# Kernel tuning notes

Hardware: AMD Instinct MI355X
Metric: run time of the kernel (lower is better)

Reference implementation:

```python
import jax, jax.numpy as jnp
import numpy as np
from jax import lax

K = 9
CENTER = K // 2
EXTEND = 1.0
EPS = 1e-5
GROUPS = 16  # out_ch // 4


def conv2d(x, w, b, stride, padding):
    y = lax.conv_general_dilated(x, w, window_strides=stride, padding=padding,
                                 dimension_numbers=('NCHW', 'OIHW', 'NCHW'))
    return y + b[None, :, None, None]


def setup_inputs() -> dict:
    key = jax.random.key(0)
    ks = jax.random.split(key, 9)
    B, C, Wd, Hd, OUT = 8, 64, 128, 128, 64
    f = jax.random.normal(ks[0], (B, C, Wd, Hd), jnp.float32)
    w_off = jax.random.normal(ks[1], (2 * K, C, 3, 3), jnp.float32) * 0.05
    b_off = jax.random.normal(ks[2], (2 * K,), jnp.float32) * 0.05
    bn_gamma = 1.0 + 0.1 * jax.random.normal(ks[3], (2 * K,), jnp.float32)
    bn_beta = 0.1 * jax.random.normal(ks[4], (2 * K,), jnp.float32)
    w_dsc = jax.random.normal(ks[5], (OUT, C, K, 1), jnp.float32) * 0.05
    b_dsc = jax.random.normal(ks[6], (OUT,), jnp.float32) * 0.05
    gn_gamma = 1.0 + 0.1 * jax.random.normal(ks[7], (OUT,), jnp.float32)
    gn_beta = 0.1 * jax.random.normal(ks[8], (OUT,), jnp.float32)
    return {'f': f, 'w_off': w_off, 'b_off': b_off, 'bn_gamma': bn_gamma,
            'bn_beta': bn_beta, 'w_dsc': w_dsc, 'b_dsc': b_dsc,
            'gn_gamma': gn_gamma, 'gn_beta': gn_beta}


def _forward(f, w_off, b_off, bn_gamma, bn_beta, w_dsc, b_dsc, gn_gamma, gn_beta):
    B, C, Wd, Hd = f.shape  # module names: width=shape[2], height=shape[3]
    dt = f.dtype

    # offset branch: conv3x3 -> BatchNorm (training mode, batch stats) -> tanh
    off = conv2d(f, w_off, b_off, (1, 1), 'SAME')
    mu = off.mean(axis=(0, 2, 3), keepdims=True)
    var = off.var(axis=(0, 2, 3), keepdims=True)
    off = (off - mu) / jnp.sqrt(var + EPS)
    off = off * bn_gamma[None, :, None, None] + bn_beta[None, :, None, None]
    off = jnp.tanh(off)

    y_off = off[:, :K]  # [B,K,Wd,Hd]; x_off (off[:, K:]) unused for morph=0

    # cumulative offset scan from the center point (morph=0).
    # NOTE: endpoints 0 and K-1 keep detached raw offsets (torch detach().clone()).
    raw0 = lax.stop_gradient(y_off)
    offn = [None] * K
    offn[CENTER] = jnp.zeros_like(y_off[:, 0])
    for i in range(1, CENTER):
        offn[CENTER + i] = offn[CENTER + i - 1] + y_off[:, CENTER + i]
        offn[CENTER - i] = offn[CENTER - i + 1] + y_off[:, CENTER - i]
    offn[0] = raw0[:, 0]
    offn[K - 1] = raw0[:, K - 1]
    offn = jnp.stack(offn, axis=1)  # [B,K,Wd,Hd]

    # coordinate grids: y indexes the width axis, x the height axis
    y_new = jnp.arange(Wd, dtype=dt)[None, None, :, None] + offn * EXTEND  # [B,K,Wd,Hd]
    x_new = ((jnp.arange(K, dtype=dt) - CENTER)[None, :, None, None]
             + jnp.arange(Hd, dtype=dt)[None, None, None, :])  # [1,K,1,Hd]
    x_new = jnp.broadcast_to(x_new, (B, K, Wd, Hd))

    # layout [B, K*Wd, Hd] via (B,K,Wd,Hd) -> (B,Wd,K,Hd)
    y_s = jnp.transpose(y_new, (0, 2, 1, 3)).reshape(B, K * Wd * Hd)
    x_s = jnp.transpose(x_new, (0, 2, 1, 3)).reshape(B, K * Wd * Hd)

    # bilinear interpolation (clamped corner indices, unclamped y/x in weights)
    y0 = jnp.floor(y_s).astype(jnp.int32)
    x0 = jnp.floor(x_s).astype(jnp.int32)
    y0c = jnp.clip(y0, 0, Wd - 1)
    y1c = jnp.clip(y0 + 1, 0, Wd - 1)
    x0c = jnp.clip(x0, 0, Hd - 1)
    x1c = jnp.clip(x0 + 1, 0, Hd - 1)

    feat = jnp.transpose(f, (0, 2, 3, 1)).reshape(B, Wd * Hd, C)

    def gather(yi, xi):
        idx = (yi * Hd + xi)[:, :, None]  # [B,N,1]
        return jnp.take_along_axis(feat, idx, axis=1)  # [B,N,C]

    va0 = gather(y0c, x0c)
    vc0 = gather(y0c, x1c)
    va1 = gather(y1c, x0c)
    vc1 = gather(y1c, x1c)

    y0f, y1f = y0c.astype(dt), y1c.astype(dt)
    x0f, x1f = x0c.astype(dt), x1c.astype(dt)
    wa = ((y1f - y_s) * (x1f - x_s))[:, :, None]
    wb = ((y1f - y_s) * (x_s - x0f))[:, :, None]
    wc = ((y_s - y0f) * (x1f - x_s))[:, :, None]
    wd = ((y_s - y0f) * (x_s - x0f))[:, :, None]

    out = va0 * wa + vc0 * wb + va1 * wc + vc1 * wd  # [B,N,C]
    deformed = jnp.transpose(out.reshape(B, K * Wd, Hd, C), (0, 3, 1, 2))  # [B,C,K*Wd,Hd]

    # strided conv over the K snake points -> [B,OUT,Wd,Hd]
    x = conv2d(deformed, w_dsc, b_dsc, (K, 1), 'VALID')

    # GroupNorm + ReLU
    OUT = x.shape[1]
    xg = x.reshape(B, GROUPS, -1)
    gmu = xg.mean(axis=-1, keepdims=True)
    gvar = xg.var(axis=-1, keepdims=True)
    xg = (xg - gmu) / jnp.sqrt(gvar + EPS)
    x = xg.reshape(x.shape) * gn_gamma[None, :, None, None] + gn_beta[None, :, None, None]
    return jax.nn.relu(x)


def reference(f, w_off, b_off, bn_gamma, bn_beta, w_dsc, b_dsc, gn_gamma, gn_beta):
    return _forward(f, w_off, b_off, bn_gamma, bn_beta, w_dsc, b_dsc, gn_gamma, gn_beta)
```

## Files before the change

### kernel.cpp

```cpp
#include <hip/hip_runtime.h>

#define B_   8
#define C_   64
#define W_   128
#define H_   128
#define K_   9
#define OUT_ 64
#define NPIX (B_*W_*H_)
#define EPS_ 1e-5f

typedef __attribute__((ext_vector_type(8))) short bf16x8;
typedef __attribute__((ext_vector_type(4))) float f32x4;

#define FEATBF_OFF  0
#define XPRE_OFF    4194304
#define OFFPRE_OFF  8388608
#define OFFH_OFF    9568256
#define WT_OFF      14286848
#define WP_OFF      14305280
#define BNSTATS_OFF 14310464
#define GSTATS_OFF  14310500
#define STATS_BYTES ((18+18+256+256)*sizeof(float))

__device__ __forceinline__ unsigned pack2bf(float a, float b) {
    union { float f; unsigned u; } ua, ub;
    ua.f = a; ub.f = b;
    unsigned x = ua.u, y = ub.u;
    x += 0x7fffu + ((x >> 16) & 1u);
    y += 0x7fffu + ((y >> 16) & 1u);
    return (x >> 16) | (y & 0xffff0000u);
}
__device__ __forceinline__ float bflo(unsigned u) {
    union { unsigned u; float f; } v; v.u = u << 16; return v.f;
}
__device__ __forceinline__ float bfhi(unsigned u) {
    union { unsigned u; float f; } v; v.u = u & 0xffff0000u; return v.f;
}

__global__ __launch_bounds__(256) void k_nhwc(const float* __restrict__ f,
                                              unsigned short* __restrict__ featbf) {
    __shared__ float tile[64][65];
    int bid = blockIdx.x;
    int ht = bid & 1;
    int w  = (bid >> 1) & 127;
    int b  = bid >> 8;
    int t  = threadIdx.x;
    int lh = t & 63;
    int c0 = (t >> 6) * 16;
    const float* fp = f + (((b*64)*128 + w)*128) + ht*64 + lh;
#pragma unroll
    for (int i = 0; i < 16; i++) {
        int c = c0 + i;
        tile[c][lh] = fp[c*16384];
    }
    __syncthreads();
    int lc = t & 63;
    int h0 = (t >> 6) * 16;
    unsigned short* obf = featbf + ((size_t)((b*128 + w)*128) + ht*64)*64 + lc;
#pragma unroll
    for (int i = 0; i < 16; i++) {
        int hr = h0 + i;
        union { float f; unsigned u; } v; v.f = tile[lc][hr];
        unsigned x = v.u + 0x7fffu + ((v.u >> 16) & 1u);
        obf[(size_t)hr*64] = (unsigned short)(x >> 16);
    }
}

__global__ void k_wprep(const float* __restrict__ w_dsc, unsigned short* __restrict__ wTbf,
                        const float* __restrict__ w_off, float* __restrict__ wP) {
    int bid = blockIdx.x;
    if (bid < 144) {
        int i = bid*256 + threadIdx.x;
        if (i >= 9*64*64) return;
        int c = i & 63;
        int o = (i >> 6) & 63;
        int k = i >> 12;
        union { float f; unsigned u; } v;
        v.f = w_dsc[(o*64 + c)*9 + k];
        unsigned x = v.u + 0x7fffu + ((v.u >> 16) & 1u);
        wTbf[i] = (unsigned short)(x >> 16);
    } else {
        int i = (bid-144)*256 + threadIdx.x;
        if (i >= 64*81) return;
        int c    = i / 81;
        int rem  = i % 81;
        int dw   = rem / 27;
        int rem2 = rem % 27;
        int ck   = rem2 / 3;
        int dh   = rem2 % 3;
        wP[i] = w_off[ck*576 + c*9 + dw*3 + dh];
    }
}

__global__ __launch_bounds__(128) void k_conv_off(const float* __restrict__ f,
                                                  const float* __restrict__ wP,
                                                  float* __restrict__ off_half) {
    int t   = threadIdx.x;
    int bid = blockIdx.x;
    int b   = bid & 7;
    int w   = (bid >> 3) & 127;
    int cq  = bid >> 10;
    int h   = t;

    float em = (h == 0)   ? 0.f : 1.f;
    float ep = (h == 127) ? 0.f : 1.f;

    const float* fb = f + (size_t)b*1048576 + (size_t)(cq*16)*16384 + (size_t)w*128;
    const float* wb = wP + cq*16*81;

    float acc[9];
#pragma unroll
    for (int ck = 0; ck < 9; ck++) acc[ck] = 0.f;

#pragma unroll 4
    for (int c = 0; c < 16; c++) {
        const float* p  = fb + c*16384;
        const float* wc = wb + c*81;
#pragma unroll
        for (int dw = -1; dw <= 1; dw++) {
            int wy = w + dw;
            if ((unsigned)wy < 128u) {
                const float* q = p + dw*128;
                float v1 = q[h];
                float v0 = __shfl_up(v1, 1);
                float v2 = __shfl_down(v1, 1);
                if (t == 64) v0 = q[63];
                if (t == 63) v2 = q[64];
                v0 *= em; v2 *= ep;
                const float* ww = wc + (dw+1)*27;
#pragma unroll
                for (int ck = 0; ck < 9; ck++)
                    acc[ck] += v0*ww[ck*3] + v1*ww[ck*3+1] + v2*ww[ck*3+2];
            }
        }
    }

    float* dst = off_half + (size_t)cq*1179648;
    int pixoff = (w << 7) + h;
#pragma unroll
    for (int ck = 0; ck < 9; ck++)
        dst[((b*9 + ck) << 14) + pixoff] = acc[ck];
}

__global__ __launch_bounds__(256) void k_bn_stats(const float* __restrict__ off_half,
                                                  float* __restrict__ off_pre,
                                                  float* __restrict__ bnstats) {
    __shared__ float wred[4][2];
    int bid = blockIdx.x;
    int b  = bid / 36;
    int rem = bid % 36;
    int ck = rem / 4;
    int wq = rem % 4;
    int t  = threadIdx.x;
    int base4 = (((b*9+ck) << 14) + wq*4096) >> 2;

    const float4* h0 = (const float4*)off_half;
    const float4* h1 = (const float4*)(off_half + 1179648);
    const float4* h2 = (const float4*)(off_half + 2359296);
    const float4* h3 = (const float4*)(off_half + 3538944);
    float4* op = (float4*)off_pre;

    float s = 0.f, q = 0.f;
#pragma unroll
    for (int i = 0; i < 4; i++) {
        int idx = base4 + t + i*256;
        float4 a = h0[idx], bb = h1[idx], cc = h2[idx], dd = h3[idx];
        float4 v;
        v.x = (a.x + bb.x) + (cc.x + dd.x);
        v.y = (a.y + bb.y) + (cc.y + dd.y);
        v.z = (a.z + bb.z) + (cc.z + dd.z);
        v.w = (a.w + bb.w) + (cc.w + dd.w);
        op[idx] = v;
        s += v.x + v.y + v.z + v.w;
        q += v.x*v.x + v.y*v.y + v.z*v.z + v.w*v.w;
    }
    for (int off = 32; off; off >>= 1) {
        s += __shfl_down(s, off);
        q += __shfl_down(q, off);
    }
    if ((t & 63) == 0) { wred[t >> 6][0] = s; wred[t >> 6][1] = q; }
    __syncthreads();
    if (t == 0) atomicAdd(&bnstats[ck*2],   wred[0][0]+wred[1][0]+wred[2][0]+wred[3][0]);
    if (t == 1) atomicAdd(&bnstats[ck*2+1], wred[0][1]+wred[1][1]+wred[2][1]+wred[3][1]);
}

__global__ __launch_bounds__(256) void k_sample_dsc(const unsigned short* __restrict__ featbf,
                                                    const float* __restrict__ off_pre,
                                                    const float* __restrict__ bnstats,
                                                    const float* __restrict__ bn_gamma,
                                                    const float* __restrict__ bn_beta,
                                                    const unsigned short* __restrict__ wTbf,
                                                    const float* __restrict__ b_dsc,
                                                    unsigned short* __restrict__ xprebf,
                                                    float* __restrict__ gstats) {
    __shared__ __align__(16) unsigned char lds_samp[64*128];
    __shared__ __align__(16) unsigned char lds_wk[64*128];
    __shared__ float ynew[9][64];
    __shared__ float red[16][2];
    __shared__ float bnab[18];

    int t = threadIdx.x;
    int bid = blockIdx.x;
    int b = bid & 7, w = (bid >> 3) & 127, mh = bid >> 10;
    int hbase = mh * 64;

    if (t < 9) {
        float n    = (float)NPIX;
        float mean = bnstats[t*2] / n;
        float var  = bnstats[t*2+1] / n - mean*mean;
        float A    = bn_gamma[t] / sqrtf(var + EPS_);
        bnab[t*2]   = A;
        bnab[t*2+1] = bn_beta[t] - mean * A;
    }
    if (t < 16) { red[t][0] = 0.f; red[t][1] = 0.f; }
    __syncthreads();

    if (t < 64) {
        int h = hbase + t;
        float y[9];
#pragma unroll
        for (int ck = 0; ck < 9; ck++) {
            float v = off_pre[((b*9+ck) << 14) + (w << 7) + h];
            y[ck] = tanhf(bnab[ck*2]*v + bnab[ck*2+1]);
        }
        float ofn[9];
        ofn[4] = 0.f;
        ofn[5] = y[5]; ofn[6] = y[5]+y[6]; ofn[7] = y[5]+y[6]+y[7];
        ofn[3] = y[3]; ofn[2] = y[3]+y[2]; ofn[1] = y[3]+y[2]+y[1];
        ofn[0] = y[0]; ofn[8] = y[8];
#pragma unroll
        for (int k = 0; k < 9; k++) ynew[k][t] = (float)w + ofn[k];
    }

    f32x4 acc[4];
#pragma unroll
    for (int ni = 0; ni < 4; ni++) {
        acc[ni][0] = 0.f; acc[ni][1] = 0.f; acc[ni][2] = 0.f; acc[ni][3] = 0.f;
    }

    int lane = t & 63, wv = t >> 6;
    int m0 = wv * 16;
    int lm = lane & 15, lk = lane >> 4;
    int hsl = t >> 2;
    int cq  = t & 3;

    uint4 wv0, wv1;
    {
        const uint4* src = (const uint4*)wTbf;
        wv0 = src[t];
        wv1 = src[t + 256];
    }

    __syncthreads();

    for (int k = 0; k < 9; k++) {
        if (k) __syncthreads();

        {
#pragma unroll
            for (int i = 0; i < 2; i++) {
                int ci = t + i*256;
                uint4 v = (i == 0) ? wv0 : wv1;
                int o  = ci >> 3;
                int cb = (ci & 7) << 4;
                *(uint4*)(lds_wk + o*128 + (cb ^ ((o & 7) << 4))) = v;
            }
        }

        {
            int hg = hbase + hsl;
            int x0 = k - 4 + hg;
            unsigned char* dst = lds_samp + hsl*128;
            int bcol0 = cq * 32;
            if ((unsigned)x0 < 127u) {
                float ys = ynew[k][hsl];
                int y0  = (int)floorf(ys);
                int y0c = min(max(y0, 0), 127), y1c = min(max(y0+1, 0), 127);
                float wa = (float)y1c - ys;
                float wc = ys - (float)y0c;
                const unsigned short* pb = featbf + ((size_t)b << 20);
                const uint4* p0 = (const uint4*)(pb + (y0c*128 + x0)*64) + cq*2;
                const uint4* p1 = (const uint4*)(pb + (y1c*128 + x0)*64) + cq*2;
#pragma unroll
                for (int ci = 0; ci < 2; ci++) {
                    uint4 a = p0[ci], c = p1[ci];
                    uint4 u;
                    u.x = pack2bf(bflo(a.x)*wa + bflo(c.x)*wc, bfhi(a.x)*wa + bfhi(c.x)*wc);
                    u.y = pack2bf(bflo(a.y)*wa + bflo(c.y)*wc, bfhi(a.y)*wa + bfhi(c.y)*wc);
                    u.z = pack2bf(bflo(a.z)*wa + bflo(c.z)*wc, bfhi(a.z)*wa + bfhi(c.z)*wc);
                    u.w = pack2bf(bflo(a.w)*wa + bflo(c.w)*wc, bfhi(a.w)*wa + bfhi(c.w)*wc);
                    *(uint4*)(dst + ((bcol0 + ci*16) ^ ((hsl & 7) << 4))) = u;
                }
            } else {
                uint4 z = make_uint4(0,0,0,0);
#pragma unroll
                for (int ci = 0; ci < 2; ci++)
                    *(uint4*)(dst + ((bcol0 + ci*16) ^ ((hsl & 7) << 4))) = z;
            }
        }

        if (k < 8) {
            const uint4* src = (const uint4*)(wTbf + ((k+1) << 12));
            wv0 = src[t];
            wv1 = src[t + 256];
        }
        __syncthreads();

#pragma unroll
        for (int ks = 0; ks < 2; ks++) {
            bf16x8 af, bfr[4];
            {
                int hl = m0 + lm;
                af = *(const bf16x8*)(lds_samp + hl*128 + ((ks*64 + lk*16) ^ ((hl & 7) << 4)));
            }
#pragma unroll
            for (int ni = 0; ni < 4; ni++) {
                int o = ni*16 + lm;
                bfr[ni] = *(const bf16x8*)(lds_wk + o*128 + ((ks*64 + lk*16) ^ ((o & 7) << 4)));
            }
#pragma unroll
            for (int ni = 0; ni < 4; ni++)
                acc[ni] = __builtin_amdgcn_mfma_f32_16x16x32_bf16(af, bfr[ni], acc[ni], 0, 0, 0);
        }
    }

#pragma unroll
    for (int ni = 0; ni < 4; ni++) {
        int o = ni*16 + lm;
        float bias = b_dsc[o];
        float4 r;
        r.x = acc[ni][0] + bias;
        r.y = acc[ni][1] + bias;
        r.z = acc[ni][2] + bias;
        r.w = acc[ni][3] + bias;
        float s1 = r.x + r.y + r.z + r.w;
        float s2 = r.x*r.x + r.y*r.y + r.z*r.z + r.w*r.w;
        int hg = hbase + m0 + lk*4;
        uint2 u2;
        u2.x = pack2bf(r.x, r.y);
        u2.y = pack2bf(r.z, r.w);
        *(uint2*)(xprebf + (((b*64 + o) << 14) + (w << 7) + hg)) = u2;

        s1 += __shfl_xor(s1, 1);  s1 += __shfl_xor(s1, 2);
        s1 += __shfl_xor(s1, 16); s1 += __shfl_xor(s1, 32);
        s2 += __shfl_xor(s2, 1);  s2 += __shfl_xor(s2, 2);
        s2 += __shfl_xor(s2, 16); s2 += __shfl_xor(s2, 32);
        if (lk == 0 && (lm & 3) == 0) {
            atomicAdd(&red[ni*4 + (lm >> 2)][0], s1);
            atomicAdd(&red[ni*4 + (lm >> 2)][1], s2);
        }
    }
    __syncthreads();
    if (t < 16) {
        atomicAdd(&gstats[(b*16 + t)*2],   red[t][0]);
        atomicAdd(&gstats[(b*16 + t)*2+1], red[t][1]);
    }
}

__global__ __launch_bounds__(256) void k_gn_apply(const unsigned short* __restrict__ xprebf,
                                                  const float* __restrict__ gstats,
                                                  const float* __restrict__ gn_gamma,
                                                  const float* __restrict__ gn_beta,
                                                  float* __restrict__ out) {
    int i8  = blockIdx.x*256 + threadIdx.x;
    int idx = i8 * 8;
    int o = (idx >> 14) & 63;
    int b = idx >> 20;
    int g = o >> 2;
    float n    = 65536.f;
    float mean = gstats[(b*16+g)*2] / n;
    float var  = gstats[(b*16+g)*2+1] / n - mean*mean;
    float istd = 1.0f / sqrtf(var + EPS_);
    float ga = gn_gamma[o] * istd;
    float be = gn_beta[o] - mean * ga;
    uint4 v = *(const uint4*)(xprebf + idx);
    float4 r0, r1;
    r0.x = fmaxf(bflo(v.x)*ga + be, 0.f);
    r0.y = fmaxf(bfhi(v.x)*ga + be, 0.f);
    r0.z = fmaxf(bflo(v.y)*ga + be, 0.f);
    r0.w = fmaxf(bfhi(v.y)*ga + be, 0.f);
    r1.x = fmaxf(bflo(v.z)*ga + be, 0.f);
    r1.y = fmaxf(bfhi(v.z)*ga + be, 0.f);
    r1.z = fmaxf(bflo(v.w)*ga + be, 0.f);
    r1.w = fmaxf(bfhi(v.w)*ga + be, 0.f);
    *(float4*)(out + idx)     = r0;
    *(float4*)(out + idx + 4) = r1;
}

extern "C" void kernel_launch(void* const* d_in, const int* in_sizes, int n_in,
                              void* d_out, int out_size, void* d_ws, size_t ws_size,
                              hipStream_t stream) {
    const float* f        = (const float*)d_in[0];
    const float* w_off    = (const float*)d_in[1];
    const float* bn_gamma = (const float*)d_in[3];
    const float* bn_beta  = (const float*)d_in[4];
    const float* w_dsc    = (const float*)d_in[5];
    const float* b_dsc    = (const float*)d_in[6];
    const float* gn_gamma = (const float*)d_in[7];
    const float* gn_beta  = (const float*)d_in[8];

    float* ws      = (float*)d_ws;
    unsigned short* featbf = (unsigned short*)(ws + FEATBF_OFF);
    unsigned short* xprebf = (unsigned short*)(ws + XPRE_OFF);
    float* off_pre = ws + OFFPRE_OFF;
    float* off_half= ws + OFFH_OFF;
    unsigned short* wTbf = (unsigned short*)(ws + WT_OFF);
    float* wP      = ws + WP_OFF;
    float* bnstats = ws + BNSTATS_OFF;
    float* gstats  = ws + GSTATS_OFF;

    hipMemsetAsync(bnstats, 0, STATS_BYTES, stream);

    k_nhwc<<<2048, 256, 0, stream>>>(f, featbf);
    k_wprep<<<165, 256, 0, stream>>>(w_dsc, wTbf, w_off, wP);
    k_conv_off<<<4096, 128, 0, stream>>>(f, wP, off_half);
    k_bn_stats<<<288, 256, 0, stream>>>(off_half, off_pre, bnstats);
    k_sample_dsc<<<2048, 256, 0, stream>>>(featbf, off_pre, bnstats, bn_gamma, bn_beta,
                                           wTbf, b_dsc, xprebf, gstats);
    k_gn_apply<<<4096, 256, 0, stream>>>(xprebf, gstats, gn_gamma, gn_beta, (float*)d_out);
}
```

Measured before the change: 125.7 us.

## Double-buffer sampled features and weights in LDS to overlap gathers with MFMA

The per-tap loop in the sample+DSC kernel now uses two LDS buffers for the sampled tile and the weight slice. Global gathers for tap k+1 are issued before the MFMAs for tap k, and the interpolated results are written to the other buffer afterwards, so there is one barrier per iteration instead of two. This is meant to hide gather latency behind matrix work, at the cost of doubling LDS use (32KB) and holding more live registers.

```diff
diff --git a/kernel.cpp b/kernel.cpp
--- a/kernel.cpp
+++ b/kernel.cpp
@@ -193,8 +193,8 @@
                                                     const float* __restrict__ b_dsc,
                                                     unsigned short* __restrict__ xprebf,
                                                     float* __restrict__ gstats) {
-    __shared__ __align__(16) unsigned char lds_samp[64*128];
-    __shared__ __align__(16) unsigned char lds_wk[64*128];
+    __shared__ __align__(16) unsigned char lds_samp[2][64*128];
+    __shared__ __align__(16) unsigned char lds_wk[2][64*128];
     __shared__ float ynew[9][64];
     __shared__ float red[16][2];
     __shared__ float bnab[18];
@@ -231,6 +231,7 @@
 #pragma unroll
         for (int k = 0; k < 9; k++) ynew[k][t] = (float)w + ofn[k];
     }
+    __syncthreads();
 
     f32x4 acc[4];
 #pragma unroll
@@ -243,84 +244,119 @@
     int lm = lane & 15, lk = lane >> 4;
     int hsl = t >> 2;
     int cq  = t & 3;
-
-    uint4 wv0, wv1;
+    const unsigned short* pbase = featbf + ((size_t)b << 20);
+
+    uint4 sa0, sa1, sb0, sb1, wv0, wv1;
+    float twa = 0.f, twc = 0.f;
+    bool valid = false;
+
     {
+        int hg = hbase + hsl;
+        int x0 = 0 - 4 + hg;
+        valid = (unsigned)x0 < 127u;
+        if (valid) {
+            float ys = ynew[0][hsl];
+            int y0  = (int)floorf(ys);
+            int y0c = min(max(y0, 0), 127), y1c = min(max(y0+1, 0), 127);
+            twa = (float)y1c - ys; twc = ys - (float)y0c;
+            const uint4* p0 = (const uint4*)(pbase + (y0c*128 + x0)*64) + cq*2;
+            const uint4* p1 = (const uint4*)(pbase + (y1c*128 + x0)*64) + cq*2;
+            sa0 = p0[0]; sa1 = p0[1];
+            sb0 = p1[0]; sb1 = p1[1];
+        }
         const uint4* src = (const uint4*)wTbf;
-        wv0 = src[t];
-        wv1 = src[t + 256];
-    }
-
+        wv0 = src[t]; wv1 = src[t + 256];
+    }
+    {
+        unsigned char* dst = lds_samp[0] + hsl*128;
+        int bcol0 = cq * 32;
+        uint4 u0 = make_uint4(0,0,0,0), u1 = make_uint4(0,0,0,0);
+        if (valid) {
+            u0.x = pack2bf(bflo(sa0.x)*twa + bflo(sb0.x)*twc, bfhi(sa0.x)*twa + bfhi(sb0.x)*twc);
+            u0.y = pack2bf(bflo(sa0.y)*twa + bflo(sb0.y)*twc, bfhi(sa0.y)*twa + bfhi(sb0.y)*twc);
+            u0.z = pack2bf(bflo(sa0.z)*twa + bflo(sb0.z)*twc, bfhi(sa0.z)*twa + bfhi(sb0.z)*twc);
+            u0.w = pack2bf(bflo(sa0.w)*twa + bflo(sb0.w)*twc, bfhi(sa0.w)*twa + bfhi(sb0.w)*twc);
+            u1.x = pack2bf(bflo(sa1.x)*twa + bflo(sb1.x)*twc, bfhi(sa1.x)*twa + bfhi(sb1.x)*twc);
+            u1.y = pack2bf(bflo(sa1.y)*twa + bflo(sb1.y)*twc, bfhi(sa1.y)*twa + bfhi(sb1.y)*twc);
+            u1.z = pack2bf(bflo(sa1.z)*twa + bflo(sb1.z)*twc, bfhi(sa1.z)*twa + bfhi(sb1.z)*twc);
+            u1.w = pack2bf(bflo(sa1.w)*twa + bflo(sb1.w)*twc, bfhi(sa1.w)*twa + bfhi(sb1.w)*twc);
+        }
+        *(uint4*)(dst + ((bcol0     ) ^ ((hsl & 7) << 4))) = u0;
+        *(uint4*)(dst + ((bcol0 + 16) ^ ((hsl & 7) << 4))) = u1;
+#pragma unroll
+        for (int i = 0; i < 2; i++) {
+            int ci = t + i*256;
+            uint4 v = (i == 0) ? wv0 : wv1;
+            int o  = ci >> 3;
+            int cb = (ci & 7) << 4;
+            *(uint4*)(lds_wk[0] + o*128 + (cb ^ ((o & 7) << 4))) = v;
+        }
+    }
     __syncthreads();
 
     for (int k = 0; k < 9; k++) {
-        if (k) __syncthreads();
-
-        {
+        int cur = k & 1, nxt = cur ^ 1;
+
+        if (k < 8) {
+            int hg = hbase + hsl;
+            int x0 = (k+1) - 4 + hg;
+            valid = (unsigned)x0 < 127u;
+            if (valid) {
+                float ys = ynew[k+1][hsl];
+                int y0  = (int)floorf(ys);
+                int y0c = min(max(y0, 0), 127), y1c = min(max(y0+1, 0), 127);
+                twa = (float)y1c - ys; twc = ys - (float)y0c;
+                const uint4* p0 = (const uint4*)(pbase + (y0c*128 + x0)*64) + cq*2;
+                const uint4* p1 = (const uint4*)(pbase + (y1c*128 + x0)*64) + cq*2;
+                sa0 = p0[0]; sa1 = p0[1];
+                sb0 = p1[0]; sb1 = p1[1];
+            }
+            const uint4* src = (const uint4*)(wTbf + ((k+1) << 12));
+            wv0 = src[t]; wv1 = src[t + 256];
+        }
+
+#pragma unroll
+        for (int ks = 0; ks < 2; ks++) {
+            bf16x8 af, bfr[4];
+            {
+                int hl = m0 + lm;
+                af = *(const bf16x8*)(lds_samp[cur] + hl*128 + ((ks*64 + lk*16) ^ ((hl & 7) << 4)));
+            }
+#pragma unroll
+            for (int ni = 0; ni < 4; ni++) {
+                int o = ni*16 + lm;
+                bfr[ni] = *(const bf16x8*)(lds_wk[cur] + o*128 + ((ks*64 + lk*16) ^ ((o & 7) << 4)));
+            }
+#pragma unroll
+            for (int ni = 0; ni < 4; ni++)
+                acc[ni] = __builtin_amdgcn_mfma_f32_16x16x32_bf16(af, bfr[ni], acc[ni], 0, 0, 0);
+        }
+
+        if (k < 8) {
+            unsigned char* dst = lds_samp[nxt] + hsl*128;
+            int bcol0 = cq * 32;
+            uint4 u0 = make_uint4(0,0,0,0), u1 = make_uint4(0,0,0,0);
+            if (valid) {
+                u0.x = pack2bf(bflo(sa0.x)*twa + bflo(sb0.x)*twc, bfhi(sa0.x)*twa + bfhi(sb0.x)*twc);
+                u0.y = pack2bf(bflo(sa0.y)*twa + bflo(sb0.y)*twc, bfhi(sa0.y)*twa + bfhi(sb0.y)*twc);
+                u0.z = pack2bf(bflo(sa0.z)*twa + bflo(sb0.z)*twc, bfhi(sa0.z)*twa + bfhi(sb0.z)*twc);
+                u0.w = pack2bf(bflo(sa0.w)*twa + bflo(sb0.w)*twc, bfhi(sa0.w)*twa + bfhi(sb0.w)*twc);
+                u1.x = pack2bf(bflo(sa1.x)*twa + bflo(sb1.x)*twc, bfhi(sa1.x)*twa + bfhi(sb1.x)*twc);
+                u1.y = pack2bf(bflo(sa1.y)*twa + bflo(sb1.y)*twc, bfhi(sa1.y)*twa + bfhi(sb1.y)*twc);
+                u1.z = pack2bf(bflo(sa1.z)*twa + bflo(sb1.z)*twc, bfhi(sa1.z)*twa + bfhi(sb1.z)*twc);
+                u1.w = pack2bf(bflo(sa1.w)*twa + bflo(sb1.w)*twc, bfhi(sa1.w)*twa + bfhi(sb1.w)*twc);
+            }
+            *(uint4*)(dst + ((bcol0     ) ^ ((hsl & 7) << 4))) = u0;
+            *(uint4*)(dst + ((bcol0 + 16) ^ ((hsl & 7) << 4))) = u1;
 #pragma unroll
             for (int i = 0; i < 2; i++) {
                 int ci = t + i*256;
                 uint4 v = (i == 0) ? wv0 : wv1;
                 int o  = ci >> 3;
                 int cb = (ci & 7) << 4;
-                *(uint4*)(lds_wk + o*128 + (cb ^ ((o & 7) << 4))) = v;
-            }
-        }
-
-        {
-            int hg = hbase + hsl;
-            int x0 = k - 4 + hg;
-            unsigned char* dst = lds_samp + hsl*128;
-            int bcol0 = cq * 32;
-            if ((unsigned)x0 < 127u) {
-                float ys = ynew[k][hsl];
-                int y0  = (int)floorf(ys);
-                int y0c = min(max(y0, 0), 127), y1c = min(max(y0+1, 0), 127);
-                float wa = (float)y1c - ys;
-                float wc = ys - (float)y0c;
-                const unsigned short* pb = featbf + ((size_t)b << 20);
-                const uint4* p0 = (const uint4*)(pb + (y0c*128 + x0)*64) + cq*2;
-                const uint4* p1 = (const uint4*)(pb + (y1c*128 + x0)*64) + cq*2;
-#pragma unroll
-                for (int ci = 0; ci < 2; ci++) {
-                    uint4 a = p0[ci], c = p1[ci];
-                    uint4 u;
-                    u.x = pack2bf(bflo(a.x)*wa + bflo(c.x)*wc, bfhi(a.x)*wa + bfhi(c.x)*wc);
-                    u.y = pack2bf(bflo(a.y)*wa + bflo(c.y)*wc, bfhi(a.y)*wa + bfhi(c.y)*wc);
-                    u.z = pack2bf(bflo(a.z)*wa + bflo(c.z)*wc, bfhi(a.z)*wa + bfhi(c.z)*wc);
-                    u.w = pack2bf(bflo(a.w)*wa + bflo(c.w)*wc, bfhi(a.w)*wa + bfhi(c.w)*wc);
-                    *(uint4*)(dst + ((bcol0 + ci*16) ^ ((hsl & 7) << 4))) = u;
-                }
-            } else {
-                uint4 z = make_uint4(0,0,0,0);
-#pragma unroll
-                for (int ci = 0; ci < 2; ci++)
-                    *(uint4*)(dst + ((bcol0 + ci*16) ^ ((hsl & 7) << 4))) = z;
-            }
-        }
-
-        if (k < 8) {
-            const uint4* src = (const uint4*)(wTbf + ((k+1) << 12));
-            wv0 = src[t];
-            wv1 = src[t + 256];
-        }
-        __syncthreads();
-
-#pragma unroll
-        for (int ks = 0; ks < 2; ks++) {
-            bf16x8 af, bfr[4];
-            {
-                int hl = m0 + lm;
-                af = *(const bf16x8*)(lds_samp + hl*128 + ((ks*64 + lk*16) ^ ((hl & 7) << 4)));
-            }
-#pragma unroll
-            for (int ni = 0; ni < 4; ni++) {
-                int o = ni*16 + lm;
-                bfr[ni] = *(const bf16x8*)(lds_wk + o*128 + ((ks*64 + lk*16) ^ ((o & 7) << 4)));
-            }
-#pragma unroll
-            for (int ni = 0; ni < 4; ni++)
-                acc[ni] = __builtin_amdgcn_mfma_f32_16x16x32_bf16(af, bfr[ni], acc[ni], 0, 0, 0);
+                *(uint4*)(lds_wk[nxt] + o*128 + (cb ^ ((o & 7) << 4))) = v;
+            }
+            __syncthreads();
         }
     }
 
```

Result: no change. 125.5 us (-0.2%).
